# Optimization experiments

Measured on AMD Instinct MI355X. Metric: run time of the kernel, lower is better.

## Reference

```python
import jax, jax.numpy as jnp
import numpy as np

BIG_DIST = 1.0e7      # replaces NaN entries of the distance matrix (torch: where(isnan, 1e7))
BIG_DIFF = 10000.0    # nan_to_num value for cyclic coordinate error
MATCH_SAMPLE_NUM = 128


def setup_inputs() -> dict:
    key = jax.random.key(0)
    k1, k2, k3, k4, k5, k6 = jax.random.split(key, 6)
    b, h, w, c = 8, 64, 64, 384
    hw = h * w
    K = MATCH_SAMPLE_NUM
    return {
        "feature1": jax.random.normal(k1, (b, h, w, c), dtype=jnp.float32),
        "feature2": jax.random.normal(k2, (b, h, w, c), dtype=jnp.float32),
        "mask1": jax.random.randint(k3, (b, h, w, 1), 0, 2).astype(jnp.int32),
        "mask2": jax.random.randint(k4, (b, h, w, 1), 0, 2).astype(jnp.int32),
        "choose_backup1": jax.random.randint(k5, (b, K), 0, hw).astype(jnp.int32),
        "choose_backup2": jax.random.randint(k6, (b, K), 0, hw).astype(jnp.int32),
    }


def _masked_cdist(feature1, feature2, m1, m2):
    """Euclidean cdist of L2-normalized features; pairs touching a masked-out
    token get BIG_DIST (equivalent to torch's NaN-fill -> isnan -> 1e7)."""
    b, h, w, c = feature1.shape
    hw = h * w
    f1 = feature1.reshape(b, hw, c)
    f2 = feature2.reshape(b, hw, c)
    f1 = f1 / jnp.linalg.norm(f1, axis=-1, keepdims=True)
    f2 = f2 / jnp.linalg.norm(f2, axis=-1, keepdims=True)
    f1 = jnp.where(m1[..., None], f1, 0.0)
    f2 = jnp.where(m2[..., None], f2, 0.0)
    sq1 = jnp.sum(f1 * f1, axis=-1)              # [b, hw]
    sq2 = jnp.sum(f2 * f2, axis=-1)              # [b, hw]
    dots = jnp.einsum("bic,bjc->bij", f1, f2)    # [b, hw, hw]
    d2 = sq1[:, :, None] + sq2[:, None, :] - 2.0 * dots
    d = jnp.sqrt(jnp.maximum(d2, 0.0))
    valid_pair = m1[:, :, None] & m2[:, None, :]
    return jnp.where(valid_pair, d, BIG_DIST)


def _cyclic_diff(match_fwd, match_bwd, m_src, m_dst, h, w):
    """Cyclic-consistency coordinate error for each source token."""
    b, hw = match_fwd.shape
    # cyclic index: src -> dst (match_fwd) -> back to src (match_bwd gathered)
    dst_valid = jnp.take_along_axis(m_dst, match_fwd, axis=1)           # [b, hw]
    cyc = jnp.take_along_axis(match_bwd, match_fwd, axis=1)             # [b, hw]
    cx = (cyc // w).astype(jnp.float32)
    cy = (cyc % w).astype(jnp.float32)
    idx = jnp.arange(hw)
    gx = (idx // w).astype(jnp.float32)[None, :]
    gy = (idx % w).astype(jnp.float32)[None, :]
    diff = jnp.sqrt((cx - gx) ** 2 + (cy - gy) ** 2)
    valid = m_src & dst_valid
    return jnp.where(valid, diff, BIG_DIFF)


def reference(feature1, feature2, mask1, mask2, choose_backup1, choose_backup2):
    b, h, w, c = feature1.shape
    hw = h * w
    K = MATCH_SAMPLE_NUM
    m1 = mask1.reshape(b, hw) > 0
    m2 = mask2.reshape(b, hw) > 0

    d = _masked_cdist(feature1, feature2, m1, m2)   # [b, hw, hw]
    match1 = jnp.argmin(d, axis=-1)                 # best j for each i, [b, hw]
    match2 = jnp.argmin(d, axis=-2)                 # best i for each j, [b, hw]

    coord_diff1 = _cyclic_diff(match1, match2, m1, m2, h, w)
    coord_diff2 = _cyclic_diff(match2, match1, m2, m1, h, w)

    choose1 = jax.lax.top_k(-coord_diff1, K)[1]
    choose1 = jnp.where((jnp.sum(m1, axis=-1) >= K)[:, None], choose1, choose_backup1)
    choose1_match = jnp.take_along_axis(match1, choose1, axis=1)

    choose2 = jax.lax.top_k(-coord_diff2, K)[1]
    choose2 = jnp.where((jnp.sum(m2, axis=-1) >= K)[:, None], choose2, choose_backup2)
    choose2_match = jnp.take_along_axis(match2, choose2, axis=1)

    out_match1 = jnp.stack([choose1, choose1_match], axis=-1)   # [b, K, 2]
    out_match2 = jnp.stack([choose2, choose2_match], axis=-1)   # [b, K, 2]
    return out_match1, out_match2
```

## Files before the change

### kernel.cpp

```cpp
#include <hip/hip_runtime.h>
#include <stdint.h>

#define HW 4096
#define CH 384
#define NB 8
#define K_SEL 128
#define BIG_DIST 1.0e7f
#define BIG_DIFF 10000.0f
#define PAGE 8192
#define NKB 12
#define NRB 32

typedef unsigned long long u64;
typedef _Float16 f16;
typedef _Float16 f16x8 __attribute__((ext_vector_type(8)));
typedef float f32x4 __attribute__((ext_vector_type(4)));

__device__ __forceinline__ u64 encode_di(float d, int idx) {
    return ((u64)__float_as_uint(d) << 32) | (unsigned)idx;
}

__device__ __forceinline__ void gl_lds16(const void* g, void* l) {
    __builtin_amdgcn_global_load_lds(
        (const __attribute__((address_space(1))) unsigned int*)g,
        (__attribute__((address_space(3))) unsigned int*)l, 16, 0, 0);
}

__device__ __forceinline__ int swz(int row, int bytecol) {
    return (row * 64 + bytecol) ^ ((row & 7) << 4);
}

__global__ __launch_bounds__(1024)
void compact_mask(const int* __restrict__ mask1, const int* __restrict__ mask2,
                  int* __restrict__ vidx1, int* __restrict__ vidx2,
                  int* __restrict__ cpos1, int* __restrict__ cpos2,
                  u64* __restrict__ slot1, u64* __restrict__ slot2,
                  int* __restrict__ cnts) {
    const int b = blockIdx.x, which = blockIdx.y;
    const int* m = (which ? mask2 : mask1) + (size_t)b * HW;
    int* vidx = (which ? vidx2 : vidx1) + (size_t)b * HW;
    int* cpos = (which ? cpos2 : cpos1) + (size_t)b * HW;
    u64* slot = (which ? slot2 : slot1) + (size_t)b * HW;
    const int tid = threadIdx.x;
    const int lane = tid & 63, wv = tid >> 6;

    const int base = tid * 4;
    int4 mm = *(const int4*)(m + base);
    int v0 = mm.x > 0, v1 = mm.y > 0, v2 = mm.z > 0, v3 = mm.w > 0;
    int sum = v0 + v1 + v2 + v3;

    int inc = sum;
#pragma unroll
    for (int off = 1; off < 64; off <<= 1) {
        int o = __shfl_up(inc, off, 64);
        if (lane >= off) inc += o;
    }
    __shared__ int wtot[16], wbase[16];
    if (lane == 63) wtot[wv] = inc;
    __syncthreads();
    if (tid == 0) {
        int acc = 0;
        for (int w = 0; w < 16; ++w) { wbase[w] = acc; acc += wtot[w]; }
        cnts[b * 2 + which] = acc;
    }
    __syncthreads();
    int pos = wbase[wv] + inc - sum;
    if (v0) { vidx[pos] = base;     cpos[base]     = pos; pos++; } else cpos[base]     = -1;
    if (v1) { vidx[pos] = base + 1; cpos[base + 1] = pos; pos++; } else cpos[base + 1] = -1;
    if (v2) { vidx[pos] = base + 2; cpos[base + 2] = pos; pos++; } else cpos[base + 2] = -1;
    if (v3) { vidx[pos] = base + 3; cpos[base + 3] = pos; pos++; } else cpos[base + 3] = -1;
    __syncthreads();
    const int cnt = wbase[15] + wtot[15];
    for (int t = cnt + tid; t < HW; t += 1024) vidx[t] = 0;
    for (int t = tid; t < HW; t += 1024) slot[t] = ~0ULL;
}

__global__ void normalize_valid(const float* __restrict__ f1,
                                const float* __restrict__ f2,
                                const int* __restrict__ vidx1,
                                const int* __restrict__ vidx2,
                                const int* __restrict__ cnts,
                                float* __restrict__ rnc1, float* __restrict__ rnc2,
                                float* __restrict__ sqc1, float* __restrict__ sqc2) {
    int gw = (blockIdx.x * blockDim.x + threadIdx.x) >> 6;
    int lane = threadIdx.x & 63;
    int which = gw >> 15;
    int rs = gw & 32767;
    int b = rs >> 12, r = rs & (HW - 1);
    const int cnt = cnts[b * 2 + which];
    float* rnc = which ? rnc2 : rnc1;
    float* sqc = which ? sqc2 : sqc1;
    const size_t bb = (size_t)b * HW;
    if (r >= cnt) {
        if (lane == 0) { rnc[bb + r] = 0.f; sqc[bb + r] = 0.f; }
        return;
    }
    const int* vidx = which ? vidx2 : vidx1;
    const float* f = which ? f2 : f1;
    const int orig = vidx[bb + r];
    const float* p = f + (bb + orig) * CH;
    float x[6];
    float s = 0.f;
#pragma unroll
    for (int t = 0; t < 6; ++t) { x[t] = p[lane + 64 * t]; s += x[t] * x[t]; }
#pragma unroll
    for (int off = 32; off >= 1; off >>= 1) s += __shfl_xor(s, off, 64);
    float rinv = 1.0f / __fsqrt_rn(s);
    float s2 = 0.f;
#pragma unroll
    for (int t = 0; t < 6; ++t) { float y = x[t] * rinv; s2 += y * y; }
#pragma unroll
    for (int off = 32; off >= 1; off >>= 1) s2 += __shfl_xor(s2, off, 64);
    if (lane == 0) { rnc[bb + r] = rinv; sqc[bb + r] = s2; }
}

__global__ __launch_bounds__(256)
void convert_tiles(const float* __restrict__ f1, const float* __restrict__ f2,
                   const float* __restrict__ rnc1, const float* __restrict__ rnc2,
                   const int* __restrict__ vidx1, const int* __restrict__ vidx2,
                   const int* __restrict__ cnts,
                   char* __restrict__ tA, char* __restrict__ tB) {
    int lin = blockIdx.x;
    int kb = lin % NKB;
    int rb = (lin / NKB) % NRB;
    int b = lin / (NKB * NRB);
    const int which = blockIdx.y;
    const int cnt = cnts[b * 2 + which];
    if (rb * 128 >= cnt) return;

    const float* f = which ? f2 : f1;
    const float* rnc = which ? rnc2 : rnc1;
    const int* vidx = (which ? vidx2 : vidx1) + (size_t)b * HW;
    char* t = which ? tB : tA;
    char* hipg = t + (size_t)lin * 2 * PAGE;
    char* lopg = hipg + PAGE;
    int rowbase = rb * 128;

#pragma unroll
    for (int p = 0; p < 4; ++p) {
        int q = p * 256 + threadIdx.x;
        int r = q >> 3;
        int kq = q & 7;
        int grow = vidx[rowbase + r];
        float rv = rnc[(size_t)b * HW + rowbase + r];
        float4 x = *(const float4*)(f + ((size_t)b * HW + grow) * CH + kb * 32 + kq * 4);
        x.x *= rv; x.y *= rv; x.z *= rv; x.w *= rv;
        f16 h0 = (f16)x.x, h1 = (f16)x.y, h2 = (f16)x.z, h3 = (f16)x.w;
        f16 l0 = (f16)((x.x - (float)h0) * 2048.0f);
        f16 l1 = (f16)((x.y - (float)h1) * 2048.0f);
        f16 l2 = (f16)((x.z - (float)h2) * 2048.0f);
        f16 l3 = (f16)((x.w - (float)h3) * 2048.0f);
        int off = swz(r, kq * 8);
        union { f16 h[4]; uint2 u; } H = {{h0, h1, h2, h3}};
        union { f16 h[4]; uint2 u; } L = {{l0, l1, l2, l3}};
        *(uint2*)(hipg + off) = H.u;
        *(uint2*)(lopg + off) = L.u;
    }
}

__global__ __launch_bounds__(256, 3)
void gemm_argmin(const char* __restrict__ tA, const char* __restrict__ tB,
                 const float* __restrict__ sqc1, const float* __restrict__ sqc2,
                 const int* __restrict__ vidx1, const int* __restrict__ vidx2,
                 const int* __restrict__ cnts,
                 u64* __restrict__ slot1, u64* __restrict__ slot2) {
    __shared__ __align__(16) char smem[4 * PAGE];
    __shared__ u64 rowSlot[128];
    __shared__ u64 colSlot[128];

    const int b = blockIdx.y;
    const int tid = threadIdx.x;

    const int cnt1 = cnts[b * 2], cnt2 = cnts[b * 2 + 1];
    const int nby = (cnt1 + 127) >> 7;
    const int nbx = (cnt2 + 127) >> 7;
    const int nact = nby * nbx;

    const int xcd = blockIdx.x & 7;
    const int s = blockIdx.x >> 3;
    const int q = nact >> 3, r8 = nact & 7;
    const int csz = q + (xcd < r8 ? 1 : 0);
    if (s >= csz) return;
    const int L = (xcd < r8 ? xcd * (q + 1) : r8 * (q + 1) + (xcd - r8) * q) + s;
    const int bx = L / nby;
    const int by = L - bx * nby;
    const int brow = by * 128, bcol = bx * 128;

    const char* Abase = tA + (size_t)(b * NRB + by) * NKB * 2 * PAGE;
    const char* Bbase = tB + (size_t)(b * NRB + bx) * NKB * 2 * PAGE;

    const int wv = tid >> 6, lane = tid & 63;
    const int wr = wv >> 1, wc = wv & 1;
    const int r0 = lane & 15, kc = lane >> 4;

    int aoff[4], boff[4];
#pragma unroll
    for (int m = 0; m < 4; ++m) {
        int ra = wr * 64 + m * 16 + r0;
        aoff[m] = swz(ra, kc * 16);
        int rb_ = wc * 64 + m * 16 + r0;
        boff[m] = swz(rb_, kc * 16);
    }

    f32x4 acc[4][4];
    f32x4 zero = {0.f, 0.f, 0.f, 0.f};
#pragma unroll
    for (int m = 0; m < 4; ++m)
#pragma unroll
        for (int n = 0; n < 4; ++n) acc[m][n] = zero;

    const int stg = wv * 1024;
    const int src_l = stg + lane * 16;
    const f16 K2048 = (f16)2048.0f;

    for (int kb = 0; kb < NKB; ++kb) {
        const char* gA = Abase + (size_t)kb * 2 * PAGE;
        const char* gB = Bbase + (size_t)kb * 2 * PAGE;
#pragma unroll
        for (int p = 0; p < 4; ++p) {
            gl_lds16(gA + p * 4096 + src_l, smem + p * 4096 + stg);
            gl_lds16(gB + p * 4096 + src_l, smem + 16384 + p * 4096 + stg);
        }
        asm volatile("s_waitcnt vmcnt(0)" ::: "memory");
        __syncthreads();

        f16x8 bh[4], bl[4];
#pragma unroll
        for (int n = 0; n < 4; ++n) {
            bh[n] = *(const f16x8*)(smem + 2 * PAGE + boff[n]);
            bl[n] = *(const f16x8*)(smem + 3 * PAGE + boff[n]);
        }
#pragma unroll
        for (int m = 0; m < 4; ++m) {
            f16x8 ah = *(const f16x8*)(smem + aoff[m]);
            f16x8 al = *(const f16x8*)(smem + PAGE + aoff[m]);
            f16x8 ah2 = ah * K2048;
#pragma unroll
            for (int n = 0; n < 4; ++n) {
                acc[m][n] = __builtin_amdgcn_mfma_f32_16x16x32_f16(ah2, bh[n], acc[m][n], 0, 0, 0);
                acc[m][n] = __builtin_amdgcn_mfma_f32_16x16x32_f16(ah, bl[n], acc[m][n], 0, 0, 0);
                acc[m][n] = __builtin_amdgcn_mfma_f32_16x16x32_f16(al, bh[n], acc[m][n], 0, 0, 0);
            }
        }
        __syncthreads();
    }

    if (tid < 128) { rowSlot[tid] = ~0ULL; colSlot[tid] = ~0ULL; }
    __syncthreads();

    const size_t bb = (size_t)b * HW;
    const int rfrag = kc * 4;
    float s1v[4][4];
    int o1v[4][4], val1[4][4];
#pragma unroll
    for (int m = 0; m < 4; ++m) {
        int rr = brow + wr * 64 + m * 16 + rfrag;
        float4 sv = *(const float4*)(sqc1 + bb + rr);
        int4 ov = *(const int4*)(vidx1 + bb + rr);
        s1v[m][0] = sv.x; s1v[m][1] = sv.y; s1v[m][2] = sv.z; s1v[m][3] = sv.w;
        o1v[m][0] = ov.x; o1v[m][1] = ov.y; o1v[m][2] = ov.z; o1v[m][3] = ov.w;
#pragma unroll
        for (int j = 0; j < 4; ++j) val1[m][j] = (rr + j) < cnt1;
    }
    float s2v[4];
    int o2v[4], val2[4];
#pragma unroll
    for (int n = 0; n < 4; ++n) {
        int cc = bcol + wc * 64 + n * 16 + r0;
        s2v[n] = sqc2[bb + cc];
        o2v[n] = vidx2[bb + cc];
        val2[n] = cc < cnt2;
    }

    u64 cbest[4] = {~0ULL, ~0ULL, ~0ULL, ~0ULL};
#pragma unroll
    for (int m = 0; m < 4; ++m) {
#pragma unroll
        for (int j = 0; j < 4; ++j) {
            u64 rbest = ~0ULL;
#pragma unroll
            for (int n = 0; n < 4; ++n) {
                float d;
                if (val1[m][j] && val2[n]) {
                    float dot = acc[m][n][j] * (1.0f / 2048.0f);
                    float t = __fmul_rn(2.0f, dot);
                    float d2 = __fsub_rn(__fadd_rn(s1v[m][j], s2v[n]), t);
                    d = __fsqrt_rn(fmaxf(d2, 0.0f));
                } else {
                    d = BIG_DIST;
                }
                u64 er = encode_di(d, o2v[n]);
                u64 ec = encode_di(d, o1v[m][j]);
                if (er < rbest) rbest = er;
                if (ec < cbest[n]) cbest[n] = ec;
            }
            atomicMin(&rowSlot[wr * 64 + m * 16 + rfrag + j], rbest);
        }
    }
#pragma unroll
    for (int n = 0; n < 4; ++n)
        atomicMin(&colSlot[wc * 64 + n * 16 + r0], cbest[n]);
    __syncthreads();

    if (tid < 128) atomicMin(&slot1[bb + brow + tid], rowSlot[tid]);
    else           atomicMin(&slot2[bb + bcol + tid - 128], colSlot[tid - 128]);
}

__global__ void scatter_matches(const u64* __restrict__ slot1,
                                const u64* __restrict__ slot2,
                                const int* __restrict__ cpos1,
                                const int* __restrict__ cpos2,
                                int* __restrict__ match1, int* __restrict__ match2) {
    int g = blockIdx.x * blockDim.x + threadIdx.x;
    if (g >= NB * HW) return;
    int b = g >> 12;
    size_t bb = (size_t)b * HW;
    int p1 = cpos1[g];
    int v1 = 0;
    if (p1 >= 0) {
        u64 sv = slot1[bb + p1];
        if (sv != ~0ULL) v1 = (int)(unsigned)(sv & 0xFFFFFFFFu);
    }
    match1[g] = v1;
    int p2 = cpos2[g];
    int v2 = 0;
    if (p2 >= 0) {
        u64 sv = slot2[bb + p2];
        if (sv != ~0ULL) v2 = (int)(unsigned)(sv & 0xFFFFFFFFu);
    }
    match2[g] = v2;
}

__global__ __launch_bounds__(1024)
void topk_output(const int* __restrict__ match1, const int* __restrict__ match2,
                 const int* __restrict__ mask1, const int* __restrict__ mask2,
                 const int* __restrict__ backup1, const int* __restrict__ backup2,
                 int* __restrict__ out) {
    __shared__ u64 keys[HW];
    __shared__ u64 sel[K_SEL];
    __shared__ int hist[256];
    __shared__ int cnt, selc, sbuck, srank;
    const int b = blockIdx.x;
    const int dir = blockIdx.y;
    const int* mF = dir ? match2 : match1;
    const int* mB = dir ? match1 : match2;
    const int* maskS = dir ? mask2 : mask1;
    const int* maskD = dir ? mask1 : mask2;
    const int* backup = dir ? backup2 : backup1;
    const int tid = threadIdx.x;
    const size_t base = (size_t)b * HW;

    if (tid == 0) { cnt = 0; selc = 0; }
    __syncthreads();
    int local = 0;
    for (int t = tid; t < HW; t += 1024) {
        int mf = mF[base + t];
        int dv = maskD[base + mf];
        int cyc = mB[base + mf];
        float gx = (float)(t >> 6), gy = (float)(t & 63);
        float dx = (float)(cyc >> 6) - gx;
        float dy = (float)(cyc & 63) - gy;
        float diff = __fsqrt_rn(dx * dx + dy * dy);
        int ms = maskS[base + t];
        float v = (ms > 0 && dv > 0) ? diff : BIG_DIFF;
        keys[t] = encode_di(v, t);
        local += (ms > 0) ? 1 : 0;
    }
    atomicAdd(&cnt, local);
    __syncthreads();

    u64 prefix = 0;
    int rank = 127;
    for (int shift = 56; shift >= 0; shift -= 8) {
        for (int h = tid; h < 256; h += 1024) hist[h] = 0;
        __syncthreads();
        for (int t = tid; t < HW; t += 1024) {
            u64 k = keys[t];
            bool match = (shift == 56) || ((k >> (shift + 8)) == prefix);
            if (match) atomicAdd(&hist[(int)((k >> shift) & 255)], 1);
        }
        __syncthreads();
        if (tid == 0) {
            int accum = 0, bkt = 0;
            for (; bkt < 256; ++bkt) {
                if (accum + hist[bkt] > rank) break;
                accum += hist[bkt];
            }
            sbuck = bkt; srank = rank - accum;
        }
        __syncthreads();
        prefix = (prefix << 8) | (unsigned)sbuck;
        rank = srank;
        __syncthreads();
    }
    const u64 pivot = prefix;

    for (int t = tid; t < HW; t += 1024) {
        u64 k = keys[t];
        if (k <= pivot) { int p = atomicAdd(&selc, 1); sel[p] = k; }
    }
    __syncthreads();

    for (unsigned kk = 2; kk <= K_SEL; kk <<= 1) {
        for (unsigned j = kk >> 1; j > 0; j >>= 1) {
            if (tid < K_SEL) {
                unsigned ixj = tid ^ j;
                if (ixj > tid) {
                    u64 a = sel[tid], c = sel[ixj];
                    bool up = ((tid & kk) == 0);
                    if ((a > c) == up) { sel[tid] = c; sel[ixj] = a; }
                }
            }
            __syncthreads();
        }
    }

    if (tid < K_SEL) {
        int c;
        if (cnt >= K_SEL) c = (int)(unsigned)(sel[tid] & 0xFFFFFFFFu);
        else c = backup[b * K_SEL + tid];
        int cm = mF[base + c];
        int* o = out + dir * (NB * K_SEL * 2);
        o[(b * K_SEL + tid) * 2 + 0] = c;
        o[(b * K_SEL + tid) * 2 + 1] = cm;
    }
}

extern "C" void kernel_launch(void* const* d_in, const int* in_sizes, int n_in,
                              void* d_out, int out_size, void* d_ws, size_t ws_size,
                              hipStream_t stream) {
    const float* f1 = (const float*)d_in[0];
    const float* f2 = (const float*)d_in[1];
    const int* mask1 = (const int*)d_in[2];
    const int* mask2 = (const int*)d_in[3];
    const int* backup1 = (const int*)d_in[4];
    const int* backup2 = (const int*)d_in[5];
    int* out = (int*)d_out;

    char* ws = (char*)d_ws;
    char* tA = ws;                    ws += (size_t)NB * NRB * NKB * 2 * PAGE;
    char* tB = ws;                    ws += (size_t)NB * NRB * NKB * 2 * PAGE;
    u64* slot1 = (u64*)ws;            ws += (size_t)NB * HW * 8;
    u64* slot2 = (u64*)ws;            ws += (size_t)NB * HW * 8;
    float* rnc1 = (float*)ws;         ws += (size_t)NB * HW * 4;
    float* rnc2 = (float*)ws;         ws += (size_t)NB * HW * 4;
    float* sqc1 = (float*)ws;         ws += (size_t)NB * HW * 4;
    float* sqc2 = (float*)ws;         ws += (size_t)NB * HW * 4;
    int* vidx1 = (int*)ws;            ws += (size_t)NB * HW * 4;
    int* vidx2 = (int*)ws;            ws += (size_t)NB * HW * 4;
    int* cpos1 = (int*)ws;            ws += (size_t)NB * HW * 4;
    int* cpos2 = (int*)ws;            ws += (size_t)NB * HW * 4;
    int* match1 = (int*)ws;           ws += (size_t)NB * HW * 4;
    int* match2 = (int*)ws;           ws += (size_t)NB * HW * 4;
    int* cnts = (int*)ws;             ws += 256;

    const int nrows = NB * HW;

    compact_mask<<<dim3(NB, 2), 1024, 0, stream>>>(mask1, mask2,
                                                   vidx1, vidx2, cpos1, cpos2,
                                                   slot1, slot2, cnts);
    normalize_valid<<<(2 * nrows) / 4, 256, 0, stream>>>(f1, f2, vidx1, vidx2,
                                                         cnts, rnc1, rnc2,
                                                         sqc1, sqc2);
    convert_tiles<<<dim3(NB * NRB * NKB, 2), 256, 0, stream>>>(f1, f2, rnc1, rnc2,
                                                               vidx1, vidx2, cnts,
                                                               tA, tB);
    gemm_argmin<<<dim3(1024, NB), 256, 0, stream>>>(tA, tB, sqc1, sqc2,
                                                    vidx1, vidx2, cnts,
                                                    slot1, slot2);
    scatter_matches<<<(nrows + 255) / 256, 256, 0, stream>>>(slot1, slot2,
                                                             cpos1, cpos2,
                                                             match1, match2);
    topk_output<<<dim3(NB, 2), 1024, 0, stream>>>(match1, match2, mask1, mask2,
                                                  backup1, backup2, out);
}
```

Baseline: 181.8 us.

## Fuse row normalization into tile conversion and parallelize radix-select bucket scan

Merges the normalize_valid and convert_tiles kernels into one prep_tiles kernel. Each block computes the inverse norms for its 128 rows, keeps them in LDS, then writes all 12 K-pages, which removes a launch and the rnc round trip through global memory. The cost is a smaller grid (512 blocks instead of 6144), serial per-wave row loops, and feature rows read twice per block. Separately, the radix-select bucket search in top-k changes from a single-thread serial scan to a 64-lane shuffle prefix scan.

```diff
diff --git a/kernel.cpp b/kernel.cpp
--- a/kernel.cpp
+++ b/kernel.cpp
@@ -75,86 +75,80 @@
     for (int t = tid; t < HW; t += 1024) slot[t] = ~0ULL;
 }
 
-__global__ void normalize_valid(const float* __restrict__ f1,
-                                const float* __restrict__ f2,
-                                const int* __restrict__ vidx1,
-                                const int* __restrict__ vidx2,
-                                const int* __restrict__ cnts,
-                                float* __restrict__ rnc1, float* __restrict__ rnc2,
-                                float* __restrict__ sqc1, float* __restrict__ sqc2) {
-    int gw = (blockIdx.x * blockDim.x + threadIdx.x) >> 6;
-    int lane = threadIdx.x & 63;
-    int which = gw >> 15;
-    int rs = gw & 32767;
-    int b = rs >> 12, r = rs & (HW - 1);
-    const int cnt = cnts[b * 2 + which];
-    float* rnc = which ? rnc2 : rnc1;
-    float* sqc = which ? sqc2 : sqc1;
-    const size_t bb = (size_t)b * HW;
-    if (r >= cnt) {
-        if (lane == 0) { rnc[bb + r] = 0.f; sqc[bb + r] = 0.f; }
-        return;
-    }
-    const int* vidx = which ? vidx2 : vidx1;
-    const float* f = which ? f2 : f1;
-    const int orig = vidx[bb + r];
-    const float* p = f + (bb + orig) * CH;
-    float x[6];
-    float s = 0.f;
-#pragma unroll
-    for (int t = 0; t < 6; ++t) { x[t] = p[lane + 64 * t]; s += x[t] * x[t]; }
-#pragma unroll
-    for (int off = 32; off >= 1; off >>= 1) s += __shfl_xor(s, off, 64);
-    float rinv = 1.0f / __fsqrt_rn(s);
-    float s2 = 0.f;
-#pragma unroll
-    for (int t = 0; t < 6; ++t) { float y = x[t] * rinv; s2 += y * y; }
-#pragma unroll
-    for (int off = 32; off >= 1; off >>= 1) s2 += __shfl_xor(s2, off, 64);
-    if (lane == 0) { rnc[bb + r] = rinv; sqc[bb + r] = s2; }
-}
-
 __global__ __launch_bounds__(256)
-void convert_tiles(const float* __restrict__ f1, const float* __restrict__ f2,
-                   const float* __restrict__ rnc1, const float* __restrict__ rnc2,
-                   const int* __restrict__ vidx1, const int* __restrict__ vidx2,
-                   const int* __restrict__ cnts,
-                   char* __restrict__ tA, char* __restrict__ tB) {
-    int lin = blockIdx.x;
-    int kb = lin % NKB;
-    int rb = (lin / NKB) % NRB;
-    int b = lin / (NKB * NRB);
+void prep_tiles(const float* __restrict__ f1, const float* __restrict__ f2,
+                const int* __restrict__ vidx1, const int* __restrict__ vidx2,
+                const int* __restrict__ cnts,
+                float* __restrict__ sqc1, float* __restrict__ sqc2,
+                char* __restrict__ tA, char* __restrict__ tB) {
+    const int lin = blockIdx.x;
+    const int rb = lin % NRB;
+    const int b = lin / NRB;
     const int which = blockIdx.y;
     const int cnt = cnts[b * 2 + which];
-    if (rb * 128 >= cnt) return;
+    const int rowbase = rb * 128;
+    if (rowbase >= cnt) return;
 
     const float* f = which ? f2 : f1;
-    const float* rnc = which ? rnc2 : rnc1;
     const int* vidx = (which ? vidx2 : vidx1) + (size_t)b * HW;
-    char* t = which ? tB : tA;
-    char* hipg = t + (size_t)lin * 2 * PAGE;
-    char* lopg = hipg + PAGE;
-    int rowbase = rb * 128;
-
-#pragma unroll
-    for (int p = 0; p < 4; ++p) {
-        int q = p * 256 + threadIdx.x;
-        int r = q >> 3;
-        int kq = q & 7;
-        int grow = vidx[rowbase + r];
-        float rv = rnc[(size_t)b * HW + rowbase + r];
-        float4 x = *(const float4*)(f + ((size_t)b * HW + grow) * CH + kb * 32 + kq * 4);
-        x.x *= rv; x.y *= rv; x.z *= rv; x.w *= rv;
-        f16 h0 = (f16)x.x, h1 = (f16)x.y, h2 = (f16)x.z, h3 = (f16)x.w;
-        f16 l0 = (f16)((x.x - (float)h0) * 2048.0f);
-        f16 l1 = (f16)((x.y - (float)h1) * 2048.0f);
-        f16 l2 = (f16)((x.z - (float)h2) * 2048.0f);
-        f16 l3 = (f16)((x.w - (float)h3) * 2048.0f);
-        int off = swz(r, kq * 8);
-        union { f16 h[4]; uint2 u; } H = {{h0, h1, h2, h3}};
-        union { f16 h[4]; uint2 u; } L = {{l0, l1, l2, l3}};
-        *(uint2*)(hipg + off) = H.u;
-        *(uint2*)(lopg + off) = L.u;
+    float* sqc = which ? sqc2 : sqc1;
+    char* pages = (which ? tB : tA) + (size_t)lin * NKB * 2 * PAGE;
+    const size_t bb = (size_t)b * HW;
+
+    __shared__ float lds_rinv[128];
+    __shared__ int lds_orig[128];
+
+    const int tid = threadIdx.x, lane = tid & 63, wv = tid >> 6;
+
+    for (int i = 0; i < 32; ++i) {
+        int rl = wv * 32 + i;
+        int r = rowbase + rl;
+        int valid = r < cnt;
+        int orig = vidx[r];
+        const float* p = f + (bb + orig) * CH;
+        float x[6];
+        float s = 0.f;
+#pragma unroll
+        for (int t = 0; t < 6; ++t) { x[t] = p[lane + 64 * t]; s += x[t] * x[t]; }
+#pragma unroll
+        for (int off = 32; off >= 1; off >>= 1) s += __shfl_xor(s, off, 64);
+        float rinv = 1.0f / __fsqrt_rn(s);
+        float s2 = 0.f;
+#pragma unroll
+        for (int t = 0; t < 6; ++t) { float y = x[t] * rinv; s2 += y * y; }
+#pragma unroll
+        for (int off = 32; off >= 1; off >>= 1) s2 += __shfl_xor(s2, off, 64);
+        if (lane == 0) {
+            lds_rinv[rl] = valid ? rinv : 0.f;
+            lds_orig[rl] = orig;
+            sqc[bb + r] = valid ? s2 : 0.f;
+        }
+    }
+    __syncthreads();
+
+    for (int kb = 0; kb < NKB; ++kb) {
+        char* hipg = pages + (size_t)kb * 2 * PAGE;
+        char* lopg = hipg + PAGE;
+#pragma unroll
+        for (int p4 = 0; p4 < 4; ++p4) {
+            int q = p4 * 256 + tid;
+            int r = q >> 3;
+            int kq = q & 7;
+            int grow = lds_orig[r];
+            float rv = lds_rinv[r];
+            float4 x = *(const float4*)(f + (bb + grow) * CH + kb * 32 + kq * 4);
+            x.x *= rv; x.y *= rv; x.z *= rv; x.w *= rv;
+            f16 h0 = (f16)x.x, h1 = (f16)x.y, h2 = (f16)x.z, h3 = (f16)x.w;
+            f16 l0 = (f16)((x.x - (float)h0) * 2048.0f);
+            f16 l1 = (f16)((x.y - (float)h1) * 2048.0f);
+            f16 l2 = (f16)((x.z - (float)h2) * 2048.0f);
+            f16 l3 = (f16)((x.w - (float)h3) * 2048.0f);
+            int off = swz(r, kq * 8);
+            union { f16 h[4]; uint2 u; } H = {{h0, h1, h2, h3}};
+            union { f16 h[4]; uint2 u; } L = {{l0, l1, l2, l3}};
+            *(uint2*)(hipg + off) = H.u;
+            *(uint2*)(lopg + off) = L.u;
+        }
     }
 }
 
@@ -380,13 +374,22 @@
             if (match) atomicAdd(&hist[(int)((k >> shift) & 255)], 1);
         }
         __syncthreads();
-        if (tid == 0) {
-            int accum = 0, bkt = 0;
-            for (; bkt < 256; ++bkt) {
-                if (accum + hist[bkt] > rank) break;
-                accum += hist[bkt];
+        if (tid < 64) {
+            int v0 = hist[tid * 4 + 0], v1 = hist[tid * 4 + 1];
+            int v2 = hist[tid * 4 + 2], v3 = hist[tid * 4 + 3];
+            int s4 = v0 + v1 + v2 + v3;
+            int inc = s4;
+#pragma unroll
+            for (int off = 1; off < 64; off <<= 1) {
+                int o = __shfl_up(inc, off, 64);
+                if (tid >= off) inc += o;
             }
-            sbuck = bkt; srank = rank - accum;
+            int c0 = inc - s4;
+            int c1 = c0 + v0, c2 = c1 + v1, c3 = c2 + v2, c4 = c3 + v3;
+            if (rank >= c0 && rank < c1)      { sbuck = tid * 4 + 0; srank = rank - c0; }
+            else if (rank >= c1 && rank < c2) { sbuck = tid * 4 + 1; srank = rank - c1; }
+            else if (rank >= c2 && rank < c3) { sbuck = tid * 4 + 2; srank = rank - c2; }
+            else if (rank >= c3 && rank < c4) { sbuck = tid * 4 + 3; srank = rank - c3; }
         }
         __syncthreads();
         prefix = (prefix << 8) | (unsigned)sbuck;
@@ -442,8 +445,6 @@
     char* tB = ws;                    ws += (size_t)NB * NRB * NKB * 2 * PAGE;
     u64* slot1 = (u64*)ws;            ws += (size_t)NB * HW * 8;
     u64* slot2 = (u64*)ws;            ws += (size_t)NB * HW * 8;
-    float* rnc1 = (float*)ws;         ws += (size_t)NB * HW * 4;
-    float* rnc2 = (float*)ws;         ws += (size_t)NB * HW * 4;
     float* sqc1 = (float*)ws;         ws += (size_t)NB * HW * 4;
     float* sqc2 = (float*)ws;         ws += (size_t)NB * HW * 4;
     int* vidx1 = (int*)ws;            ws += (size_t)NB * HW * 4;
@@ -459,12 +460,8 @@
     compact_mask<<<dim3(NB, 2), 1024, 0, stream>>>(mask1, mask2,
                                                    vidx1, vidx2, cpos1, cpos2,
                                                    slot1, slot2, cnts);
-    normalize_valid<<<(2 * nrows) / 4, 256, 0, stream>>>(f1, f2, vidx1, vidx2,
-                                                         cnts, rnc1, rnc2,
-                                                         sqc1, sqc2);
-    convert_tiles<<<dim3(NB * NRB * NKB, 2), 256, 0, stream>>>(f1, f2, rnc1, rnc2,
-                                                               vidx1, vidx2, cnts,
-                                                               tA, tB);
+    prep_tiles<<<dim3(NB * NRB, 2), 256, 0, stream>>>(f1, f2, vidx1, vidx2,
+                                                      cnts, sqc1, sqc2, tA, tB);
     gemm_argmin<<<dim3(1024, NB), 256, 0, stream>>>(tA, tB, sqc1, sqc2,
                                                     vidx1, vidx2, cnts,
                                                     slot1, slot2);
```

Result: slower. 187.4 us (+3.1%).
